# Performance work log

Hardware: AMD Instinct MI355X
Metric: run time of the kernel (lower is better)

Reference implementation:

```python
import jax, jax.numpy as jnp
import numpy as np

# config (matches SS2Dv2 defaults: d_model=96, d_state=16, ssm_ratio=2.0, dt_rank=auto=6, k_group=4)
DM, DI, N, K, R = 96, 192, 16, 4, 6
BSZ, H_, W_ = 1, 56, 56


def setup_inputs() -> dict:
    key = jax.random.key(0)
    ks = jax.random.split(key, 8)
    return {
        "x": jax.random.normal(ks[0], (BSZ, H_, W_, DM), jnp.float32),
        "in_proj_w": jax.random.normal(ks[1], (2 * DI, DM), jnp.float32) / np.sqrt(DM).astype(np.float32),
        "conv_w": jax.random.normal(ks[2], (DI, 1, 3, 3), jnp.float32) * 0.1,
        "conv_b": jnp.zeros((DI,), jnp.float32),
        "x_proj_w": jax.random.normal(ks[3], (K, R + 2 * N, DI), jnp.float32) / np.sqrt(DI).astype(np.float32),
        "dt_projs_w": 0.1 * jax.random.uniform(ks[4], (K, DI, R), jnp.float32),
        "dt_projs_bias": 0.1 * jax.random.uniform(ks[5], (K, DI), jnp.float32),
        "A_logs": jnp.zeros((K * DI, N), jnp.float32),
        "Ds": jnp.ones((K * DI,), jnp.float32),
        "ln_w": jnp.ones((DI,), jnp.float32),
        "ln_b": jnp.zeros((DI,), jnp.float32),
        "out_proj_w": jax.random.normal(ks[6], (DM, DI), jnp.float32) / np.sqrt(DI).astype(np.float32),
    }


def _cross_scan(x):
    # x: (B, D, H, W) -> (B, 4, D, L); dirs: row-major, col-major, and their flips
    B, D, H, W = x.shape
    L = H * W
    x0 = x.reshape(B, D, L)
    x1 = jnp.swapaxes(x, 2, 3).reshape(B, D, L)
    return jnp.stack([x0, x1, x0[..., ::-1], x1[..., ::-1]], axis=1)


def _cross_merge(ys, H, W):
    # ys: (B, K, D, L) -> (B, D, L); invert each scan direction and sum
    B, Kk, D, L = ys.shape
    y0 = ys[:, 0]
    y2 = ys[:, 2][..., ::-1]
    y1 = jnp.swapaxes(ys[:, 1].reshape(B, D, W, H), 2, 3).reshape(B, D, L)
    y3 = jnp.swapaxes(ys[:, 3][..., ::-1].reshape(B, D, W, H), 2, 3).reshape(B, D, L)
    return y0 + y1 + y2 + y3


def _forward(x, in_proj_w, conv_w, conv_b, x_proj_w, dt_projs_w, dt_projs_bias,
             A_logs, Ds, ln_w, ln_b, out_proj_w):
    B, H, W, _ = x.shape
    L = H * W
    # in_proj + gate split (channel_first=False -> last dim)
    xz = jnp.einsum('bhwc,oc->bhwo', x, in_proj_w)
    xc, z = jnp.split(xz, 2, axis=-1)
    z = jax.nn.silu(z)
    # depthwise conv (NCHW)
    xc = jnp.transpose(xc, (0, 3, 1, 2))
    xc = jax.lax.conv_general_dilated(
        xc, conv_w, (1, 1), 'SAME', feature_group_count=DI,
        dimension_numbers=('NCHW', 'OIHW', 'NCHW')) + conv_b[None, :, None, None]
    xc = jax.nn.silu(xc)
    # 4-directional cross scan
    xs = _cross_scan(xc)  # (B,K,D,L)
    # grouped x_proj: per direction D -> R+2N
    x_dbl = jnp.einsum('bkdl,krd->bkrl', xs, x_proj_w)
    dts, Bs, Cs = jnp.split(x_dbl, [R, R + N], axis=2)  # (B,K,R,L),(B,K,N,L),(B,K,N,L)
    # grouped dt proj: per direction R -> D
    dts = jnp.einsum('bkrl,kdr->bkdl', dts, dt_projs_w)
    A = -jnp.exp(A_logs.astype(jnp.float32)).reshape(K, DI, N)
    delta = jax.nn.softplus(dts + dt_projs_bias[None, :, :, None])  # (B,K,D,L)
    # S6 selective scan: h_t = exp(delta*A)*h_{t-1} + delta*B*u, y_t = C.h_t + D*u
    dA = jnp.exp(jnp.einsum('bkdl,kdn->bkdln', delta, A))
    dBu = jnp.einsum('bkdl,bknl,bkdl->bkdln', delta, Bs, xs)

    def comb(e1, e2):
        a1, b1 = e1
        a2, b2 = e2
        return a2 * a1, a2 * b1 + b2

    _, h = jax.lax.associative_scan(comb, (dA, dBu), axis=3)  # (B,K,D,L,N)
    y = jnp.einsum('bkdln,bknl->bkdl', h, Cs) + Ds.reshape(K, DI)[None, :, :, None] * xs
    y = _cross_merge(y, H, W).reshape(B, DI, H, W)
    # out_norm: LayerNorm over channels (channel_first=False path)
    y = jnp.transpose(y, (0, 2, 3, 1))  # (B,H,W,D)
    mu = y.mean(-1, keepdims=True)
    var = ((y - mu) ** 2).mean(-1, keepdims=True)
    y = (y - mu) / jnp.sqrt(var + 1e-5) * ln_w + ln_b
    y = y * z
    return jnp.einsum('bhwd,od->bhwo', y, out_proj_w)


def reference(x, in_proj_w, conv_w, conv_b, x_proj_w, dt_projs_w, dt_projs_bias,
              A_logs, Ds, ln_w, ln_b, out_proj_w):
    return _forward(x, in_proj_w, conv_w, conv_b, x_proj_w, dt_projs_w, dt_projs_bias,
                    A_logs, Ds, ln_w, ln_b, out_proj_w)
```

## Files before the change

kernel.cpp:

```cpp
#include <hip/hip_runtime.h>
#include <hip/hip_bf16.h>
#include <math.h>

#define DM 96
#define DI 192
#define NS 16
#define KK 4
#define RR 6
#define HH 56
#define WW 56
#define LL (HH*WW)
#define RN (RR + 2*NS)
#define NCH 64
#define CLL (LL/NCH)

__device__ __forceinline__ float silu_f(float x) { return x / (1.f + __expf(-x)); }
__device__ __forceinline__ float softplus_f(float x) {
    return (x > 20.f) ? x : log1pf(__expf(x));
}

__global__ __launch_bounds__(256) void k_inproj(
        const float* __restrict__ x, const float* __restrict__ w,
        float* __restrict__ xc_t, float* __restrict__ z_nat) {
    __shared__ float xt[32 * 100];
    __shared__ float wt[32 * 100];
    const int l0 = blockIdx.x * 32;
    const int o0 = blockIdx.y * 32;
    const int tid = threadIdx.x;
    for (int i = tid; i < 32 * 24; i += 256) {
        int r = i / 24, q = i % 24;
        *(float4*)&xt[r * 100 + 4 * q] = *(const float4*)&x[(size_t)(l0 + r) * DM + 4 * q];
        *(float4*)&wt[r * 100 + 4 * q] = *(const float4*)&w[(size_t)(o0 + r) * DM + 4 * q];
    }
    __syncthreads();
    const int tx = tid & 15, ty = tid >> 4;
    float acc[2][2] = {};
    for (int c = 0; c < 96; c += 4) {
        float4 av[2], bv[2];
#pragma unroll
        for (int i = 0; i < 2; ++i) av[i] = *(const float4*)&xt[(ty + 16 * i) * 100 + c];
#pragma unroll
        for (int j = 0; j < 2; ++j) bv[j] = *(const float4*)&wt[(tx + 16 * j) * 100 + c];
#pragma unroll
        for (int i = 0; i < 2; ++i)
#pragma unroll
            for (int j = 0; j < 2; ++j) {
                acc[i][j] = fmaf(av[i].x, bv[j].x, acc[i][j]);
                acc[i][j] = fmaf(av[i].y, bv[j].y, acc[i][j]);
                acc[i][j] = fmaf(av[i].z, bv[j].z, acc[i][j]);
                acc[i][j] = fmaf(av[i].w, bv[j].w, acc[i][j]);
            }
    }
    __syncthreads();
    float* ot = xt;
#pragma unroll
    for (int j = 0; j < 2; ++j)
#pragma unroll
        for (int i = 0; i < 2; ++i)
            ot[(tx + 16 * j) * 65 + (ty + 16 * i)] = acc[i][j];
    __syncthreads();
    if (o0 < DI) {
        for (int i = tid; i < 32 * 32; i += 256) {
            int ol = i >> 5, ll = i & 31;
            xc_t[(size_t)(o0 + ol) * LL + l0 + ll] = ot[ol * 65 + ll];
        }
    } else {
        for (int i = tid; i < 32 * 32; i += 256) {
            int ll = i >> 5, ol = i & 31;
            z_nat[(size_t)(l0 + ll) * DI + (o0 - DI) + ol] = silu_f(ot[ol * 65 + ll]);
        }
    }
}

__global__ __launch_bounds__(256) void k_convT(
        const float* __restrict__ xc_t, const float* __restrict__ cw,
        const float* __restrict__ cb, float* __restrict__ xconv, float* __restrict__ xs1) {
    __shared__ float in_s[16 * 56];
    __shared__ float out_s[14 * 57];
    const int d = blockIdx.x;
    const int h0 = blockIdx.y * 14;
    const int tid = threadIdx.x;
    const float* in = xc_t + (size_t)d * LL;
    for (int i = tid; i < 16 * 14; i += 256) {
        int row = i / 14, q = i % 14;
        int r = row - 1 + h0;
        float4 v = make_float4(0.f, 0.f, 0.f, 0.f);
        if (r >= 0 && r < HH) v = *(const float4*)&in[r * WW + 4 * q];
        *(float4*)&in_s[row * 56 + 4 * q] = v;
    }
    __syncthreads();
    const float b0 = cb[d];
    float w9[9];
#pragma unroll
    for (int i = 0; i < 9; ++i) w9[i] = cw[d * 9 + i];
    for (int i = tid; i < 14 * 56; i += 256) {
        int hh = i / 56, w = i % 56;
        float acc = b0;
#pragma unroll
        for (int di = 0; di < 3; ++di)
#pragma unroll
            for (int dj = 0; dj < 3; ++dj) {
                int w2 = w + dj - 1;
                if (w2 < 0 || w2 >= WW) continue;
                acc = fmaf(in_s[(hh + di) * 56 + w2], w9[di * 3 + dj], acc);
            }
        acc = silu_f(acc);
        xconv[(size_t)d * LL + (h0 + hh) * WW + w] = acc;
        out_s[hh * 57 + w] = acc;
    }
    __syncthreads();
    for (int i = tid; i < 14 * 56; i += 256) {
        int w = i / 14, hh = i % 14;
        xs1[(size_t)d * LL + w * HH + h0 + hh] = out_s[hh * 57 + w];
    }
}

__global__ __launch_bounds__(256) void k_xdblD(
        const float* __restrict__ xconv, const float* __restrict__ xs1,
        const float* __restrict__ pw, const float* __restrict__ dtw,
        const float* __restrict__ dtb,
        float* __restrict__ Bn, float* __restrict__ Cn, float* __restrict__ delta) {
    __shared__ float xt[DI * 16];
    __shared__ float wk_s[32 * DI];
    __shared__ float dtS[RR * 17];
    const int k = blockIdx.y;
    const int l0 = blockIdx.x * 16;
    const int tid = threadIdx.x;
    const float* in = (k & 1) ? xs1 : xconv;
    const float* wk = pw + (size_t)k * RN * DI;
    for (int i = tid; i < DI * 4; i += 256) {
        int d = i >> 2, q = i & 3;
        *(float4*)&xt[(d << 4) + 4 * q] = *(const float4*)&in[(size_t)d * LL + l0 + 4 * q];
    }
    {
        const float4* src = (const float4*)(wk + RR * DI);
        float4* dst = (float4*)wk_s;
        for (int i = tid; i < (32 * DI) / 4; i += 256) dst[i] = src[i];
    }
    __syncthreads();
    if (tid < RR * 16) {
        int r = tid >> 4, lx = tid & 15;
        const float* wr = wk + r * DI;
        float acc = 0.f;
#pragma unroll 8
        for (int d = 0; d < DI; ++d) acc = fmaf(xt[(d << 4) + lx], wr[d], acc);
        dtS[r * 17 + lx] = acc;
    }
    {
        const int sx = tid & 15, cg = tid >> 4;
        float acc2[2] = {};
        for (int d = 0; d < DI; d += 4) {
            float x0 = xt[(d + 0) * 16 + sx];
            float x1 = xt[(d + 1) * 16 + sx];
            float x2 = xt[(d + 2) * 16 + sx];
            float x3 = xt[(d + 3) * 16 + sx];
#pragma unroll
            for (int j = 0; j < 2; ++j) {
                float4 wv = *(const float4*)&wk_s[(cg + 16 * j) * DI + d];
                acc2[j] = fmaf(x0, wv.x, acc2[j]);
                acc2[j] = fmaf(x1, wv.y, acc2[j]);
                acc2[j] = fmaf(x2, wv.z, acc2[j]);
                acc2[j] = fmaf(x3, wv.w, acc2[j]);
            }
        }
        int s = l0 + sx;
        Bn[((size_t)k * LL + s) * NS + cg] = acc2[0];
        Cn[((size_t)k * LL + s) * NS + cg] = acc2[1];
    }
    __syncthreads();
    for (int oi = tid; oi < DI * 16; oi += 256) {
        int d = oi >> 4, sl = oi & 15;
        int kd = k * DI + d;
        const float* wr = dtw + (size_t)kd * RR;
        float acc = dtb[kd];
#pragma unroll
        for (int r = 0; r < RR; ++r) acc = fmaf(dtS[r * 17 + sl], wr[r], acc);
        delta[(size_t)kd * LL + l0 + sl] = softplus_f(acc);
    }
}

template<int STP, bool TRANS>
__device__ __forceinline__ void scan_dir(
        const float* __restrict__ pd, const float* __restrict__ pu,
        const float* __restrict__ pB, const float* __restrict__ pC,
        float An0, float An1, float Dv, int c, int n,
        float* __restrict__ sP, float* __restrict__ sH,
        float* __restrict__ yo0,
        float* __restrict__ ysm,
        int im0) {
    float sd = 0.f, h0 = 0.f, h1 = 0.f;
#pragma unroll 7
    for (int tl = 0; tl < CLL; ++tl) {
        float dl = pd[STP * tl];
        float u  = pu[STP * tl];
        float B0 = pB[STP * NS * tl];
        float B1 = pB[STP * NS * tl + 8];
        float dA0 = __expf(dl * An0);
        float dA1 = __expf(dl * An1);
        float du = dl * u;
        h0 = fmaf(dA0, h0, du * B0);
        h1 = fmaf(dA1, h1, du * B1);
        sd += dl;
    }
    sP[c * NS + n]     = __expf(sd * An0);
    sP[c * NS + n + 8] = __expf(sd * An1);
    sH[c * NS + n]     = h0;
    sH[c * NS + n + 8] = h1;
    __syncthreads();
    float hin0 = 0.f, hin1 = 0.f;
    for (int cc = 0; cc < c; ++cc) {
        hin0 = fmaf(sP[cc * NS + n],     hin0, sH[cc * NS + n]);
        hin1 = fmaf(sP[cc * NS + n + 8], hin1, sH[cc * NS + n + 8]);
    }

    float h20 = hin0, h21 = hin1;
    float yreg[7];
#pragma unroll 7
    for (int tl = 0; tl < CLL; ++tl) {
        float dl = pd[STP * tl];
        float u  = pu[STP * tl];
        float B0 = pB[STP * NS * tl];
        float B1 = pB[STP * NS * tl + 8];
        float C0 = pC[STP * NS * tl];
        float C1 = pC[STP * NS * tl + 8];
        float dA0 = __expf(dl * An0);
        float dA1 = __expf(dl * An1);
        float du = dl * u;
        h20 = fmaf(dA0, h20, du * B0);
        h21 = fmaf(dA1, h21, du * B1);
        float acc = h20 * C0 + h21 * C1;
        acc += __shfl_xor(acc, 4, 64);
        acc += __shfl_xor(acc, 2, 64);
        acc += __shfl_xor(acc, 1, 64);
        acc = fmaf(Dv, u, acc);
        if ((tl & 7) == n) yreg[tl >> 3] = acc;
    }
    if (!TRANS) {
#pragma unroll
        for (int j = 0; j < 6; ++j)
            yo0[STP * (j * 8 + n)] = yreg[j];
        if (n == 0)
            yo0[STP * 48] = yreg[6];
    } else {
#pragma unroll
        for (int j = 0; j < 6; ++j) {
            int im = im0 + STP * (j * 8 + n);
            int w = im / HH, hh = im - w * HH;
            ysm[hh * 57 + w] = yreg[j];
        }
        if (n == 0) {
            int im = im0 + STP * 48;
            int w = im / HH, hh = im - w * HH;
            ysm[hh * 57 + w] = yreg[6];
        }
    }
}

__global__ __launch_bounds__(512) void k_scan(
        const float* __restrict__ delta, const float* __restrict__ Bn,
        const float* __restrict__ Cn,
        const float* __restrict__ xconv, const float* __restrict__ xs1,
        const float* __restrict__ A_logs, const float* __restrict__ Ds,
        float* __restrict__ y4) {
    __shared__ float sP[NCH * NS];
    __shared__ float sH[NCH * NS];
    __shared__ float ys[HH * 57];
    int b = blockIdx.x;
    int k = b / DI, d = b % DI;
    int tid = threadIdx.x;
    int c = tid >> 3, n = tid & 7;
    int kd = k * DI + d;
    float An0 = -__expf(A_logs[kd * NS + n]);
    float An1 = -__expf(A_logs[kd * NS + n + 8]);
    float Dv = Ds[kd];
    const float* del = delta + (size_t)kd * LL;
    const float* uP  = ((k & 1) ? xs1 : xconv) + (size_t)d * LL;
    const float* Bb  = Bn + (size_t)k * LL * NS;
    const float* Cb  = Cn + (size_t)k * LL * NS;
    float* yo = y4 + (size_t)kd * LL;
    const int t0 = c * CLL;
    const int imF = t0;
    const int imR = LL - 1 - t0;
    if (k == 0) {
        scan_dir<1, false>(del + imF, uP + imF,
                           Bb + (size_t)imF * NS + n, Cb + (size_t)imF * NS + n,
                           An0, An1, Dv, c, n, sP, sH, yo + imF, nullptr, 0);
    } else if (k == 1) {
        scan_dir<1, true>(del + imF, uP + imF,
                          Bb + (size_t)imF * NS + n, Cb + (size_t)imF * NS + n,
                          An0, An1, Dv, c, n, sP, sH, nullptr, ys, imF);
    } else if (k == 2) {
        scan_dir<-1, false>(del + imR, uP + imR,
                            Bb + (size_t)imR * NS + n, Cb + (size_t)imR * NS + n,
                            An0, An1, Dv, c, n, sP, sH, yo + imR, nullptr, 0);
    } else {
        scan_dir<-1, true>(del + imR, uP + imR,
                           Bb + (size_t)imR * NS + n, Cb + (size_t)imR * NS + n,
                           An0, An1, Dv, c, n, sP, sH, nullptr, ys, imR);
    }
    if (k & 1) {
        __syncthreads();
        for (int p = tid; p < LL; p += 512)
            yo[p] = ys[p + p / WW];
    }
}

__global__ __launch_bounds__(256) void k_lnout(
        const float* __restrict__ y4, const float* __restrict__ z_nat,
        const float* __restrict__ lnw, const float* __restrict__ lnb,
        const float* __restrict__ ow, float* __restrict__ out) {
    __shared__ float yv[16 * 196];
    __shared__ float ow_s[48 * 196];
    __shared__ float mean_s[16], inv_s[16];
    const int l0 = blockIdx.x * 16;
    const int tid = threadIdx.x;
    for (int i = tid; i < DI * 4; i += 256) {
        int d = i >> 2, q = i & 3;
        size_t off = (size_t)d * LL + l0 + 4 * q;
        float4 a = *(const float4*)&y4[off];
        float4 b = *(const float4*)&y4[(size_t)DI * LL + off];
        float4 c2 = *(const float4*)&y4[(size_t)(2 * DI) * LL + off];
        float4 e = *(const float4*)&y4[(size_t)(3 * DI) * LL + off];
        int p = 4 * q;
        yv[(p + 0) * 196 + d] = a.x + b.x + c2.x + e.x;
        yv[(p + 1) * 196 + d] = a.y + b.y + c2.y + e.y;
        yv[(p + 2) * 196 + d] = a.z + b.z + c2.z + e.z;
        yv[(p + 3) * 196 + d] = a.w + b.w + c2.w + e.w;
    }
    __syncthreads();
    {
        int p = tid >> 4, e = tid & 15;
        float s1 = 0.f;
#pragma unroll
        for (int m = 0; m < 12; ++m) s1 += yv[p * 196 + e + 16 * m];
        s1 += __shfl_xor(s1, 8, 64);
        s1 += __shfl_xor(s1, 4, 64);
        s1 += __shfl_xor(s1, 2, 64);
        s1 += __shfl_xor(s1, 1, 64);
        float mean = s1 * (1.f / DI);
        float s2 = 0.f;
#pragma unroll
        for (int m = 0; m < 12; ++m) {
            float dv = yv[p * 196 + e + 16 * m] - mean;
            s2 = fmaf(dv, dv, s2);
        }
        s2 += __shfl_xor(s2, 8, 64);
        s2 += __shfl_xor(s2, 4, 64);
        s2 += __shfl_xor(s2, 2, 64);
        s2 += __shfl_xor(s2, 1, 64);
        if (e == 0) {
            mean_s[p] = mean;
            inv_s[p] = rsqrtf(s2 * (1.f / DI) + 1e-5f);
        }
    }
    __syncthreads();
    for (int i = tid; i < 16 * 48; i += 256) {
        int p = i / 48, q = i % 48;
        float4 z4 = *(const float4*)&z_nat[(size_t)(l0 + p) * DI + 4 * q];
        float4 w4 = *(const float4*)&lnw[4 * q];
        float4 b4 = *(const float4*)&lnb[4 * q];
        float4 yy = *(const float4*)&yv[p * 196 + 4 * q];
        float m = mean_s[p], iv = inv_s[p];
        yy.x = ((yy.x - m) * iv * w4.x + b4.x) * z4.x;
        yy.y = ((yy.y - m) * iv * w4.y + b4.y) * z4.y;
        yy.z = ((yy.z - m) * iv * w4.z + b4.z) * z4.z;
        yy.w = ((yy.w - m) * iv * w4.w + b4.w) * z4.w;
        *(float4*)&yv[p * 196 + 4 * q] = yy;
    }
    const int ty = tid >> 4, tx = tid & 15;
#pragma unroll
    for (int pass = 0; pass < 2; ++pass) {
        __syncthreads();
        for (int i = tid; i < 48 * 48; i += 256) {
            int o = i / 48, q = i % 48;
            *(float4*)&ow_s[o * 196 + 4 * q] =
                *(const float4*)&ow[(size_t)(pass * 48 + o) * DI + 4 * q];
        }
        __syncthreads();
        float acc[3] = {};
        for (int dd = 0; dd < DI; dd += 4) {
            float4 a0 = *(const float4*)&yv[ty * 196 + dd];
#pragma unroll
            for (int j = 0; j < 3; ++j) {
                float4 bv = *(const float4*)&ow_s[(tx + 16 * j) * 196 + dd];
                acc[j] += a0.x * bv.x + a0.y * bv.y + a0.z * bv.z + a0.w * bv.w;
            }
        }
#pragma unroll
        for (int j = 0; j < 3; ++j)
            out[(size_t)(l0 + ty) * DM + pass * 48 + tx + 16 * j] = acc[j];
    }
}

extern "C" void kernel_launch(void* const* d_in, const int* in_sizes, int n_in,
                              void* d_out, int out_size, void* d_ws, size_t ws_size,
                              hipStream_t stream) {
    const float* x    = (const float*)d_in[0];
    const float* ipw  = (const float*)d_in[1];
    const float* cw   = (const float*)d_in[2];
    const float* cb   = (const float*)d_in[3];
    const float* xpw  = (const float*)d_in[4];
    const float* dtw  = (const float*)d_in[5];
    const float* dtb  = (const float*)d_in[6];
    const float* alog = (const float*)d_in[7];
    const float* Dsp  = (const float*)d_in[8];
    const float* lnw  = (const float*)d_in[9];
    const float* lnb  = (const float*)d_in[10];
    const float* ow   = (const float*)d_in[11];
    float* out = (float*)d_out;

    float* ws     = (float*)d_ws;
    float* xc_t   = ws;
    float* z_nat  = xc_t + DI * LL;
    float* xconv  = z_nat + DI * LL;
    float* xs1    = xconv + DI * LL;
    float* Bn     = xs1 + DI * LL;
    float* Cn     = Bn + (size_t)KK * LL * NS;
    float* delta  = Cn + (size_t)KK * LL * NS;
    float* y4     = delta + (size_t)KK * DI * LL;

    k_inproj <<<dim3(LL / 32, 12), 256, 0, stream>>>(x, ipw, xc_t, z_nat);
    k_convT  <<<dim3(DI, 4), 256, 0, stream>>>(xc_t, cw, cb, xconv, xs1);
    k_xdblD  <<<dim3(LL / 16, KK), 256, 0, stream>>>(xconv, xs1, xpw, dtw, dtb, Bn, Cn, delta);
    k_scan   <<<KK * DI, 512, 0, stream>>>(delta, Bn, Cn, xconv, xs1, alog, Dsp, y4);
    k_lnout  <<<LL / 16, 256, 0, stream>>>(y4, z_nat, lnw, lnb, ow, out);
}
```

Measured before the change: 177.2 us.

## Give each scan thread four states with float4 loads and exp2

```diff
diff --git a/kernel.cpp b/kernel.cpp
--- a/kernel.cpp
+++ b/kernel.cpp
@@ -183,80 +183,84 @@
 __device__ __forceinline__ void scan_dir(
         const float* __restrict__ pd, const float* __restrict__ pu,
         const float* __restrict__ pB, const float* __restrict__ pC,
-        float An0, float An1, float Dv, int c, int n,
+        float4 An, float Dv, int c, int n,
         float* __restrict__ sP, float* __restrict__ sH,
         float* __restrict__ yo0,
         float* __restrict__ ysm,
         int im0) {
-    float sd = 0.f, h0 = 0.f, h1 = 0.f;
+    float sd = 0.f;
+    float4 h = make_float4(0.f, 0.f, 0.f, 0.f);
 #pragma unroll 7
     for (int tl = 0; tl < CLL; ++tl) {
         float dl = pd[STP * tl];
         float u  = pu[STP * tl];
-        float B0 = pB[STP * NS * tl];
-        float B1 = pB[STP * NS * tl + 8];
-        float dA0 = __expf(dl * An0);
-        float dA1 = __expf(dl * An1);
+        float4 Bv = *(const float4*)&pB[STP * NS * tl];
         float du = dl * u;
-        h0 = fmaf(dA0, h0, du * B0);
-        h1 = fmaf(dA1, h1, du * B1);
+        h.x = fmaf(__builtin_amdgcn_exp2f(dl * An.x), h.x, du * Bv.x);
+        h.y = fmaf(__builtin_amdgcn_exp2f(dl * An.y), h.y, du * Bv.y);
+        h.z = fmaf(__builtin_amdgcn_exp2f(dl * An.z), h.z, du * Bv.z);
+        h.w = fmaf(__builtin_amdgcn_exp2f(dl * An.w), h.w, du * Bv.w);
         sd += dl;
     }
-    sP[c * NS + n]     = __expf(sd * An0);
-    sP[c * NS + n + 8] = __expf(sd * An1);
-    sH[c * NS + n]     = h0;
-    sH[c * NS + n + 8] = h1;
-    __syncthreads();
-    float hin0 = 0.f, hin1 = 0.f;
+    *(float4*)&sP[c * NS + 4 * n] = make_float4(
+        __builtin_amdgcn_exp2f(sd * An.x), __builtin_amdgcn_exp2f(sd * An.y),
+        __builtin_amdgcn_exp2f(sd * An.z), __builtin_amdgcn_exp2f(sd * An.w));
+    *(float4*)&sH[c * NS + 4 * n] = h;
+    __syncthreads();
+    float4 hin = make_float4(0.f, 0.f, 0.f, 0.f);
     for (int cc = 0; cc < c; ++cc) {
-        hin0 = fmaf(sP[cc * NS + n],     hin0, sH[cc * NS + n]);
-        hin1 = fmaf(sP[cc * NS + n + 8], hin1, sH[cc * NS + n + 8]);
-    }
-
-    float h20 = hin0, h21 = hin1;
-    float yreg[7];
+        float4 P  = *(const float4*)&sP[cc * NS + 4 * n];
+        float4 Hh = *(const float4*)&sH[cc * NS + 4 * n];
+        hin.x = fmaf(P.x, hin.x, Hh.x);
+        hin.y = fmaf(P.y, hin.y, Hh.y);
+        hin.z = fmaf(P.z, hin.z, Hh.z);
+        hin.w = fmaf(P.w, hin.w, Hh.w);
+    }
+
+    float4 h2 = hin;
+    float yreg[13];
 #pragma unroll 7
     for (int tl = 0; tl < CLL; ++tl) {
         float dl = pd[STP * tl];
         float u  = pu[STP * tl];
-        float B0 = pB[STP * NS * tl];
-        float B1 = pB[STP * NS * tl + 8];
-        float C0 = pC[STP * NS * tl];
-        float C1 = pC[STP * NS * tl + 8];
-        float dA0 = __expf(dl * An0);
-        float dA1 = __expf(dl * An1);
+        float4 Bv = *(const float4*)&pB[STP * NS * tl];
+        float4 Cv = *(const float4*)&pC[STP * NS * tl];
         float du = dl * u;
-        h20 = fmaf(dA0, h20, du * B0);
-        h21 = fmaf(dA1, h21, du * B1);
-        float acc = h20 * C0 + h21 * C1;
-        acc += __shfl_xor(acc, 4, 64);
+        h2.x = fmaf(__builtin_amdgcn_exp2f(dl * An.x), h2.x, du * Bv.x);
+        h2.y = fmaf(__builtin_amdgcn_exp2f(dl * An.y), h2.y, du * Bv.y);
+        h2.z = fmaf(__builtin_amdgcn_exp2f(dl * An.z), h2.z, du * Bv.z);
+        h2.w = fmaf(__builtin_amdgcn_exp2f(dl * An.w), h2.w, du * Bv.w);
+        float acc = h2.x * Cv.x;
+        acc = fmaf(h2.y, Cv.y, acc);
+        acc = fmaf(h2.z, Cv.z, acc);
+        acc = fmaf(h2.w, Cv.w, acc);
         acc += __shfl_xor(acc, 2, 64);
         acc += __shfl_xor(acc, 1, 64);
         acc = fmaf(Dv, u, acc);
-        if ((tl & 7) == n) yreg[tl >> 3] = acc;
+        if ((tl & 3) == n) yreg[tl >> 2] = acc;
     }
     if (!TRANS) {
 #pragma unroll
-        for (int j = 0; j < 6; ++j)
-            yo0[STP * (j * 8 + n)] = yreg[j];
+        for (int j = 0; j < 12; ++j)
+            yo0[STP * (j * 4 + n)] = yreg[j];
         if (n == 0)
-            yo0[STP * 48] = yreg[6];
+            yo0[STP * 48] = yreg[12];
     } else {
 #pragma unroll
-        for (int j = 0; j < 6; ++j) {
-            int im = im0 + STP * (j * 8 + n);
+        for (int j = 0; j < 12; ++j) {
+            int im = im0 + STP * (j * 4 + n);
             int w = im / HH, hh = im - w * HH;
             ysm[hh * 57 + w] = yreg[j];
         }
         if (n == 0) {
             int im = im0 + STP * 48;
             int w = im / HH, hh = im - w * HH;
-            ysm[hh * 57 + w] = yreg[6];
-        }
-    }
-}
-
-__global__ __launch_bounds__(512) void k_scan(
+            ysm[hh * 57 + w] = yreg[12];
+        }
+    }
+}
+
+__global__ __launch_bounds__(256) void k_scan(
         const float* __restrict__ delta, const float* __restrict__ Bn,
         const float* __restrict__ Cn,
         const float* __restrict__ xconv, const float* __restrict__ xs1,
@@ -268,10 +272,12 @@
     int b = blockIdx.x;
     int k = b / DI, d = b % DI;
     int tid = threadIdx.x;
-    int c = tid >> 3, n = tid & 7;
+    int c = tid >> 2, n = tid & 3;
     int kd = k * DI + d;
-    float An0 = -__expf(A_logs[kd * NS + n]);
-    float An1 = -__expf(A_logs[kd * NS + n + 8]);
+    const float LOG2E = 1.4426950408889634f;
+    float4 Alg = *(const float4*)&A_logs[kd * NS + 4 * n];
+    float4 An = make_float4(-__expf(Alg.x) * LOG2E, -__expf(Alg.y) * LOG2E,
+                            -__expf(Alg.z) * LOG2E, -__expf(Alg.w) * LOG2E);
     float Dv = Ds[kd];
     const float* del = delta + (size_t)kd * LL;
     const float* uP  = ((k & 1) ? xs1 : xconv) + (size_t)d * LL;
@@ -283,24 +289,24 @@
     const int imR = LL - 1 - t0;
     if (k == 0) {
         scan_dir<1, false>(del + imF, uP + imF,
-                           Bb + (size_t)imF * NS + n, Cb + (size_t)imF * NS + n,
-                           An0, An1, Dv, c, n, sP, sH, yo + imF, nullptr, 0);
+                           Bb + (size_t)imF * NS + 4 * n, Cb + (size_t)imF * NS + 4 * n,
+                           An, Dv, c, n, sP, sH, yo + imF, nullptr, 0);
     } else if (k == 1) {
         scan_dir<1, true>(del + imF, uP + imF,
-                          Bb + (size_t)imF * NS + n, Cb + (size_t)imF * NS + n,
-                          An0, An1, Dv, c, n, sP, sH, nullptr, ys, imF);
+                          Bb + (size_t)imF * NS + 4 * n, Cb + (size_t)imF * NS + 4 * n,
+                          An, Dv, c, n, sP, sH, nullptr, ys, imF);
     } else if (k == 2) {
         scan_dir<-1, false>(del + imR, uP + imR,
-                            Bb + (size_t)imR * NS + n, Cb + (size_t)imR * NS + n,
-                            An0, An1, Dv, c, n, sP, sH, yo + imR, nullptr, 0);
+                            Bb + (size_t)imR * NS + 4 * n, Cb + (size_t)imR * NS + 4 * n,
+                            An, Dv, c, n, sP, sH, yo + imR, nullptr, 0);
     } else {
         scan_dir<-1, true>(del + imR, uP + imR,
-                           Bb + (size_t)imR * NS + n, Cb + (size_t)imR * NS + n,
-                           An0, An1, Dv, c, n, sP, sH, nullptr, ys, imR);
+                           Bb + (size_t)imR * NS + 4 * n, Cb + (size_t)imR * NS + 4 * n,
+                           An, Dv, c, n, sP, sH, nullptr, ys, imR);
     }
     if (k & 1) {
         __syncthreads();
-        for (int p = tid; p < LL; p += 512)
+        for (int p = tid; p < LL; p += 256)
             yo[p] = ys[p + p / WW];
     }
 }
@@ -422,6 +428,6 @@
     k_inproj <<<dim3(LL / 32, 12), 256, 0, stream>>>(x, ipw, xc_t, z_nat);
     k_convT  <<<dim3(DI, 4), 256, 0, stream>>>(xc_t, cw, cb, xconv, xs1);
     k_xdblD  <<<dim3(LL / 16, KK), 256, 0, stream>>>(xconv, xs1, xpw, dtw, dtb, Bn, Cn, delta);
-    k_scan   <<<KK * DI, 512, 0, stream>>>(delta, Bn, Cn, xconv, xs1, alog, Dsp, y4);
+    k_scan   <<<KK * DI, 256, 0, stream>>>(delta, Bn, Cn, xconv, xs1, alog, Dsp, y4);
     k_lnout  <<<LL / 16, 256, 0, stream>>>(y4, z_nat, lnw, lnb, ow, out);
 }
```

New measurement: 184.6 us. +4.2%, slower.
